# Kernel optimization log

Hardware: AMD Instinct MI355X
Metric: run time of the kernel (lower is better)

The kernel has to match this reference:

```python
import jax, jax.numpy as jnp
import numpy as np

N_NODES = 50000
N_EDGES = 800000


def gat_conv(x, src, dst, ea, W, We, a_s, a_d, a_e, b, n_nodes):
    """PyG GATConv with edge_dim, add_self_loops=True, fill_value='mean', concat=True."""
    H, C = a_s.shape
    dt = x.dtype
    # self-loop edge_attr = mean of incoming edge attrs per destination node
    deg = jax.ops.segment_sum(jnp.ones((src.shape[0],), dt), dst, num_segments=n_nodes)
    loop_attr = jax.ops.segment_sum(ea, dst, num_segments=n_nodes) / jnp.clip(deg, 1.0)[:, None]
    nodes = jnp.arange(n_nodes, dtype=src.dtype)
    s = jnp.concatenate([src, nodes])
    d = jnp.concatenate([dst, nodes])
    e_attr = jnp.concatenate([ea, loop_attr], axis=0)       # [E2, edge_dim]
    h = (x @ W).reshape(n_nodes, H, C)                       # [N,H,C]
    e = (e_attr @ We).reshape(-1, H, C)                      # [E2,H,C]
    a_src = jnp.einsum('nhc,hc->nh', h, a_s)                 # [N,H]
    a_dst = jnp.einsum('nhc,hc->nh', h, a_d)
    a_edg = jnp.einsum('ehc,hc->eh', e, a_e)                 # [E2,H]
    lg = jax.nn.leaky_relu(a_src[s] + a_dst[d] + a_edg, 0.2)  # [E2,H]
    m = jax.ops.segment_max(lg, d, num_segments=n_nodes)     # every node has a self-loop
    p = jnp.exp(lg - m[d])
    z = jax.ops.segment_sum(p, d, num_segments=n_nodes)
    alpha = p / z[d]                                         # segment softmax over dst
    out = jax.ops.segment_sum(alpha[:, :, None] * h[s], d, num_segments=n_nodes)
    return out.reshape(n_nodes, H * C) + b


def setup_inputs() -> dict:
    key = jax.random.key(0)
    ks = iter(jax.random.split(key, 40))
    sc = 0.05
    inp = {
        'x': jax.random.normal(next(ks), (N_NODES, 128), jnp.float32),
        'edge_index': jax.random.randint(next(ks), (2, N_EDGES), 0, N_NODES, dtype=jnp.int32),
        'edge_attr': jax.random.uniform(next(ks), (N_EDGES, 1), jnp.float32),
        'fa_w': jax.random.normal(next(ks), (128, 128)) * sc, 'fa_b': jnp.zeros((128,)),
        'W1': jax.random.normal(next(ks), (128, 256)) * sc, 'We1': jax.random.normal(next(ks), (1, 256)) * sc,
        'as1': jax.random.normal(next(ks), (4, 64)) * sc, 'ad1': jax.random.normal(next(ks), (4, 64)) * sc,
        'ae1': jax.random.normal(next(ks), (4, 64)) * sc, 'b1': jnp.zeros((256,)),
        'W2': jax.random.normal(next(ks), (256, 256)) * sc, 'We2': jax.random.normal(next(ks), (1, 256)) * sc,
        'as2': jax.random.normal(next(ks), (4, 64)) * sc, 'ad2': jax.random.normal(next(ks), (4, 64)) * sc,
        'ae2': jax.random.normal(next(ks), (4, 64)) * sc, 'b2': jnp.zeros((256,)),
        'W3': jax.random.normal(next(ks), (256, 64)) * sc, 'We3': jax.random.normal(next(ks), (1, 64)) * sc,
        'as3': jax.random.normal(next(ks), (1, 64)) * sc, 'ad3': jax.random.normal(next(ks), (1, 64)) * sc,
        'ae3': jax.random.normal(next(ks), (1, 64)) * sc, 'b3': jnp.zeros((64,)),
        'r1_w': jax.random.normal(next(ks), (128, 256)) * sc, 'r1_b': jnp.zeros((256,)),
        'r2_w': jax.random.normal(next(ks), (256, 256)) * sc, 'r2_b': jnp.zeros((256,)),
        'ffn_w1': jax.random.normal(next(ks), (128, 64)) * sc, 'ffn_b1': jnp.zeros((64,)),
        'ffn_w2': jax.random.normal(next(ks), (64, 64)) * sc, 'ffn_b2': jnp.zeros((64,)),
    }
    return inp


def reference(x, edge_index, edge_attr, fa_w, fa_b,
              W1, We1, as1, ad1, ae1, b1,
              W2, We2, as2, ad2, ae2, b2,
              W3, We3, as3, ad3, ae3, b3,
              r1_w, r1_b, r2_w, r2_b,
              ffn_w1, ffn_b1, ffn_w2, ffn_b2):
    n = x.shape[0]
    src, dst = edge_index[0], edge_index[1]
    # feature attention gate
    x = x * jax.nn.sigmoid(x @ fa_w + fa_b)
    xr1 = x @ r1_w + r1_b
    z1 = gat_conv(x, src, dst, edge_attr, W1, We1, as1, ad1, ae1, b1, n)
    z1 = jax.nn.leaky_relu(z1, 0.01) + xr1          # dropout = identity (eval)
    z2 = gat_conv(z1, src, dst, edge_attr, W2, We2, as2, ad2, ae2, b2, n)
    z2 = jax.nn.leaky_relu(z2, 0.01) + (z1 @ r2_w + r2_b)
    z3 = gat_conv(z2, src, dst, edge_attr, W3, We3, as3, ad3, ae3, b3, n)
    z_self = jax.nn.relu(x @ ffn_w1 + ffn_b1) @ ffn_w2 + ffn_b2
    z3 = jax.nn.leaky_relu(z3, 0.01) + z_self
    return z3
```

## Files before the change

### kernel.cpp

```cpp
#include <hip/hip_runtime.h>
#include <hip/hip_bf16.h>


typedef unsigned short u16;
typedef unsigned int   u32;
typedef __attribute__((ext_vector_type(8))) short short8;
typedef __attribute__((ext_vector_type(4))) float float4v;

typedef const __attribute__((address_space(1))) u32* gptr_t;
typedef __attribute__((address_space(3))) u32* lptr_t;
#define GLOAD_LDS16(g, l) \
    __builtin_amdgcn_global_load_lds((gptr_t)(const void*)(g), (lptr_t)(void*)(l), 16, 0, 0)

static __device__ __forceinline__ u16 f2b(float f) {
    u32 u = __float_as_uint(f);
    u32 r = u + 0x7fffu + ((u >> 16) & 1u);
    return (u16)(r >> 16);
}
static __device__ __forceinline__ float b2f(u16 u) {
    return __uint_as_float(((u32)u) << 16);
}
static __device__ __forceinline__ float lo2f(u32 v) { return __uint_as_float(v << 16); }
static __device__ __forceinline__ float hi2f(u32 v) { return __uint_as_float(v & 0xffff0000u); }
static __device__ __forceinline__ float lrelu02(float x) { return fmaxf(x, 0.2f * x); }

__global__ void prep_mega(const float* __restrict__ x, u16* __restrict__ xb, int n4,
                          const float* s0, const float* s1, const float* s2,
                          const float* s3, const float* s4, const float* s5,
                          const float* s6, const float* s7,
                          u16* d0, u16* d1, u16* d2, u16* d3,
                          u16* d4, u16* d5, u16* d6, u16* d7,
                          const float* We1, const float* ae1,
                          const float* We2, const float* ae2,
                          const float* We3, const float* ae3, float* ce_g) {
    int role = blockIdx.y;
    if (role == 0) {
        int i = blockIdx.x * 256 + threadIdx.x;
        if (i >= n4) return;
        float4 v = ((const float4*)x)[i];
        ushort4 o;
        o.x = f2b(v.x); o.y = f2b(v.y); o.z = f2b(v.z); o.w = f2b(v.w);
        ((ushort4*)xb)[i] = o;
    } else {
        int wid = blockIdx.x >> 4, sub = blockIdx.x & 15;
        if (wid > 8) return;
        if (wid == 8) {
            if (sub == 0) {
                int t = threadIdx.x;
                if (t < 9) {
                    const float* W; const float* a; int h;
                    if (t < 4)      { W = We1; a = ae1; h = t; }
                    else if (t < 8) { W = We2; a = ae2; h = t - 4; }
                    else            { W = We3; a = ae3; h = 0; }
                    float s = 0.f;
                    for (int c = 0; c < 64; c++) s += W[h * 64 + c] * a[h * 64 + c];
                    ce_g[t] = s;
                }
            }
            return;
        }
        const float* src; u16* dst; int K, N;
        switch (wid) {
            case 0: src = s0; dst = d0; K = 128; N = 128; break;
            case 1: src = s1; dst = d1; K = 128; N = 256; break;
            case 2: src = s2; dst = d2; K = 128; N = 256; break;
            case 3: src = s3; dst = d3; K = 256; N = 256; break;
            case 4: src = s4; dst = d4; K = 256; N = 256; break;
            case 5: src = s5; dst = d5; K = 256; N = 64;  break;
            case 6: src = s6; dst = d6; K = 128; N = 64;  break;
            default: src = s7; dst = d7; K = 64;  N = 64;  break;
        }
        int KN = K * N;
        int nmask = N - 1;
        int nshift = __popc((u32)nmask);
        for (int i = sub * 256 + threadIdx.x; i < KN; i += 16 * 256) {
            int k = i >> nshift, n2 = i & nmask;
            dst[(size_t)n2 * K + k] = f2b(src[i]);
        }
    }
}

__global__ void scan_block_kernel(const u32* __restrict__ deg, int* incl,
                                  int* blocksum, int Nn) {
    __shared__ int sb[256];
    int t = threadIdx.x;
    int n = blockIdx.x * 256 + t;
    int v = (n < Nn) ? (int)deg[n] : 0;
    sb[t] = v;
    __syncthreads();
    for (int off = 1; off < 256; off <<= 1) {
        int x = (t >= off) ? sb[t - off] : 0;
        __syncthreads();
        sb[t] += x;
        __syncthreads();
    }
    if (n < Nn) incl[n] = sb[t];
    if (t == 255) blocksum[blockIdx.x] = sb[255];
}

__global__ void scan_final_kernel(const u32* __restrict__ deg, const int* __restrict__ incl,
                                  const int* __restrict__ blocksum,
                                  int* row_ptr, int Nn) {
    __shared__ int sb[256];
    int t = threadIdx.x;
    int b = blockIdx.x;
    sb[t] = (t < b) ? blocksum[t] : 0;
    __syncthreads();
    for (int off = 128; off > 0; off >>= 1) {
        if (t < off) sb[t] += sb[t + off];
        __syncthreads();
    }
    int base = sb[0];
    int n = b * 256 + t;
    if (n >= Nn) return;
    int d = (int)deg[n];
    int excl = base + incl[n] - d;
    row_ptr[n] = excl;
    if (n == Nn - 1) row_ptr[Nn] = excl + d;
}

#define LDSS 40
__global__ __launch_bounds__(256)
void fa_atomic_kernel(const u16* __restrict__ A, const u16* __restrict__ Bt,
                      const float* __restrict__ bias, const u16* __restrict__ extraB,
                      u16* __restrict__ Cb,
                      const int* __restrict__ ei, u32* deg, u32* rank, int E, int nx) {
    int gid = blockIdx.x;
    int role = gid % 3;
    int idx = gid / 3;
    if (role == 2) {
        for (int e = idx * 256 + threadIdx.x; e < E; e += nx * 256)
            rank[e] = atomicAdd(&deg[ei[E + e]], 1u);
        return;
    }
    __shared__ u16 As[64 * LDSS];
    __shared__ u16 Bs[64 * LDSS];
    const int K = 128, N = 128;
    int t = threadIdx.x;
    int bm = idx * 64, bn = role * 64;
    int w = t >> 6, lane = t & 63;
    int wm = w & 1, wn = w >> 1;
    int lm = lane & 15, q = lane >> 4;

    float4v acc[2][2];
#pragma unroll
    for (int i = 0; i < 2; i++)
#pragma unroll
        for (int j = 0; j < 2; j++) acc[i][j] = (float4v){0.f, 0.f, 0.f, 0.f};

    int ar = t >> 2;
    int ac = (t & 3) * 8;
    const u16* aPtr = A + (size_t)(bm + ar) * K + ac;
    const u16* bPtr = Bt + (size_t)(bn + ar) * K + ac;

#pragma unroll
    for (int k0 = 0; k0 < K; k0 += 32) {
        uint4 av = *(const uint4*)(aPtr + k0);
        uint4 bv = *(const uint4*)(bPtr + k0);
        *(uint4*)&As[ar * LDSS + ac] = av;
        *(uint4*)&Bs[ar * LDSS + ac] = bv;
        __syncthreads();

        short8 fa0 = *(const short8*)&As[(32 * wm + lm) * LDSS + q * 8];
        short8 fa1 = *(const short8*)&As[(32 * wm + 16 + lm) * LDSS + q * 8];
        short8 fb0 = *(const short8*)&Bs[(32 * wn + lm) * LDSS + q * 8];
        short8 fb1 = *(const short8*)&Bs[(32 * wn + 16 + lm) * LDSS + q * 8];
        acc[0][0] = __builtin_amdgcn_mfma_f32_16x16x32_bf16(fa0, fb0, acc[0][0], 0, 0, 0);
        acc[0][1] = __builtin_amdgcn_mfma_f32_16x16x32_bf16(fa0, fb1, acc[0][1], 0, 0, 0);
        acc[1][0] = __builtin_amdgcn_mfma_f32_16x16x32_bf16(fa1, fb0, acc[1][0], 0, 0, 0);
        acc[1][1] = __builtin_amdgcn_mfma_f32_16x16x32_bf16(fa1, fb1, acc[1][1], 0, 0, 0);
        __syncthreads();
    }

#pragma unroll
    for (int i = 0; i < 2; i++)
#pragma unroll
        for (int j = 0; j < 2; j++) {
            int col = bn + 32 * wn + 16 * j + lm;
            float bval = bias[col];
#pragma unroll
            for (int r = 0; r < 4; r++) {
                int row = bm + 32 * wm + 16 * i + q * 4 + r;
                float v = acc[i][j][r] + bval;
                float xv = b2f(extraB[(size_t)row * N + col]);
                v = xv / (1.f + __expf(-v));
                Cb[(size_t)row * N + col] = f2b(v);
            }
        }
}

__global__ __launch_bounds__(256)
void c1_scatter_kernel(const u16* __restrict__ A, const u16* __restrict__ Bt,
                       const float* __restrict__ bias1, const float* __restrict__ bias2,
                       u16* __restrict__ Cres, u16* __restrict__ Ch, u16* __restrict__ Cmid,
                       const int* __restrict__ ei, const float* __restrict__ ea,
                       const int* __restrict__ row_ptr, const u32* __restrict__ rank,
                       int2* __restrict__ csr2, int E, int nx) {
    int gid = blockIdx.x;
    int role = gid % 6;
    int idx = gid / 6;
    if (role == 5) {
        for (int e = idx * 256 + threadIdx.x; e < E; e += nx * 256) {
            int d = ei[E + e];
            csr2[row_ptr[d] + (int)rank[e]] = make_int2(ei[e], __float_as_int(ea[e]));
        }
        return;
    }
    __shared__ u16 As[128 * 32];
    __shared__ u16 Bs[128 * 32];
    const int K = 128;
    int t = threadIdx.x;
    int w = t >> 6, lane = t & 63;
    int wm = w & 1, wn = w >> 1;
    int lm = lane & 15, q = lane >> 4;
    int bm = idx * 128, bn = role * 128;

    float4v acc[4][4];
#pragma unroll
    for (int i = 0; i < 4; i++)
#pragma unroll
        for (int j = 0; j < 4; j++) acc[i][j] = (float4v){0.f, 0.f, 0.f, 0.f};

    int srow = lane >> 2;
    int scol = (lane & 3) * 8;
    const u16* aG = A + (size_t)(bm + w * 32 + srow) * K + scol;
    const u16* bG = Bt + (size_t)(bn + w * 32 + srow) * K + scol;
    u16* aL0 = &As[(w * 32) * 32];
    u16* aL1 = &As[(w * 32 + 16) * 32];
    u16* bL0 = &Bs[(w * 32) * 32];
    u16* bL1 = &Bs[(w * 32 + 16) * 32];

#pragma unroll
    for (int k0 = 0; k0 < K; k0 += 32) {
        GLOAD_LDS16(aG + k0, aL0);
        GLOAD_LDS16(aG + (size_t)16 * K + k0, aL1);
        GLOAD_LDS16(bG + k0, bL0);
        GLOAD_LDS16(bG + (size_t)16 * K + k0, bL1);
        __syncthreads();

        short8 af[4], bf[4];
#pragma unroll
        for (int i = 0; i < 4; i++)
            af[i] = *(const short8*)&As[(64 * wm + 16 * i + lm) * 32 + q * 8];
#pragma unroll
        for (int j = 0; j < 4; j++)
            bf[j] = *(const short8*)&Bs[(64 * wn + 16 * j + lm) * 32 + q * 8];
#pragma unroll
        for (int i = 0; i < 4; i++)
#pragma unroll
            for (int j = 0; j < 4; j++)
                acc[i][j] = __builtin_amdgcn_mfma_f32_16x16x32_bf16(af[i], bf[j], acc[i][j], 0, 0, 0);
        __syncthreads();
    }

#pragma unroll
    for (int i = 0; i < 4; i++)
#pragma unroll
        for (int j = 0; j < 4; j++) {
            int col = bn + 64 * wn + 16 * j + lm;
#pragma unroll
            for (int r = 0; r < 4; r++) {
                int row = bm + 64 * wm + 16 * i + q * 4 + r;
                float v = acc[i][j][r];
                if (col < 256) {
                    Cres[(size_t)row * 256 + col] = f2b(v + bias1[col]);
                } else if (col < 512) {
                    Ch[(size_t)row * 256 + (col - 256)] = f2b(v);
                } else if (col < 576) {
                    Cmid[(size_t)row * 64 + (col - 512)] = f2b(fmaxf(v + bias2[col - 512], 0.f));
                }
            }
        }
}

template <int K>
__global__ __launch_bounds__(256)
void gemm128_kernel(const u16* __restrict__ A, const u16* __restrict__ Bt,
                    const float* __restrict__ bias1,
                    u16* __restrict__ Cres, u16* __restrict__ Ch) {
    __shared__ u16 As[128 * 32];
    __shared__ u16 Bs[128 * 32];
    int t = threadIdx.x;
    int w = t >> 6, lane = t & 63;
    int wm = w & 1, wn = w >> 1;
    int lm = lane & 15, q = lane >> 4;
    int bm = blockIdx.x * 128, bn = blockIdx.y * 128;

    float4v acc[4][4];
#pragma unroll
    for (int i = 0; i < 4; i++)
#pragma unroll
        for (int j = 0; j < 4; j++) acc[i][j] = (float4v){0.f, 0.f, 0.f, 0.f};

    int srow = lane >> 2;
    int scol = (lane & 3) * 8;
    const u16* aG = A + (size_t)(bm + w * 32 + srow) * K + scol;
    const u16* bG = Bt + (size_t)(bn + w * 32 + srow) * K + scol;
    u16* aL0 = &As[(w * 32) * 32];
    u16* aL1 = &As[(w * 32 + 16) * 32];
    u16* bL0 = &Bs[(w * 32) * 32];
    u16* bL1 = &Bs[(w * 32 + 16) * 32];

#pragma unroll
    for (int k0 = 0; k0 < K; k0 += 32) {
        GLOAD_LDS16(aG + k0, aL0);
        GLOAD_LDS16(aG + (size_t)16 * K + k0, aL1);
        GLOAD_LDS16(bG + k0, bL0);
        GLOAD_LDS16(bG + (size_t)16 * K + k0, bL1);
        __syncthreads();

        short8 af[4], bf[4];
#pragma unroll
        for (int i = 0; i < 4; i++)
            af[i] = *(const short8*)&As[(64 * wm + 16 * i + lm) * 32 + q * 8];
#pragma unroll
        for (int j = 0; j < 4; j++)
            bf[j] = *(const short8*)&Bs[(64 * wn + 16 * j + lm) * 32 + q * 8];
#pragma unroll
        for (int i = 0; i < 4; i++)
#pragma unroll
            for (int j = 0; j < 4; j++)
                acc[i][j] = __builtin_amdgcn_mfma_f32_16x16x32_bf16(af[i], bf[j], acc[i][j], 0, 0, 0);
        __syncthreads();
    }

#pragma unroll
    for (int i = 0; i < 4; i++)
#pragma unroll
        for (int j = 0; j < 4; j++) {
            int col = bn + 64 * wn + 16 * j + lm;
#pragma unroll
            for (int r = 0; r < 4; r++) {
                int row = bm + 64 * wm + 16 * i + q * 4 + r;
                float v = acc[i][j][r];
                if (col < 256) {
                    Cres[(size_t)row * 256 + col] = f2b(v + bias1[col]);
                } else {
                    Ch[(size_t)row * 256 + (col - 256)] = f2b(v);
                }
            }
        }
}

template <int EPI, int K>
__global__ __launch_bounds__(256)
void gemm_kernel(const u16* __restrict__ A, const u16* __restrict__ Bt,
                 const float* __restrict__ bias, u16* __restrict__ Cb, int N) {
    __shared__ u16 As[64 * LDSS];
    __shared__ u16 Bs[64 * LDSS];
    int t = threadIdx.x;
    int bm = blockIdx.x * 64, bn = blockIdx.y * 64;
    int w = t >> 6, lane = t & 63;
    int wm = w & 1, wn = w >> 1;
    int lm = lane & 15, q = lane >> 4;

    float4v acc[2][2];
#pragma unroll
    for (int i = 0; i < 2; i++)
#pragma unroll
        for (int j = 0; j < 2; j++) acc[i][j] = (float4v){0.f, 0.f, 0.f, 0.f};

    int ar = t >> 2;
    int ac = (t & 3) * 8;
    const u16* aPtr = A + (size_t)(bm + ar) * K + ac;
    const u16* bPtr = Bt + (size_t)(bn + ar) * K + ac;

#pragma unroll
    for (int k0 = 0; k0 < K; k0 += 32) {
        uint4 av = *(const uint4*)(aPtr + k0);
        uint4 bv = *(const uint4*)(bPtr + k0);
        *(uint4*)&As[ar * LDSS + ac] = av;
        *(uint4*)&Bs[ar * LDSS + ac] = bv;
        __syncthreads();

        short8 fa0 = *(const short8*)&As[(32 * wm + lm) * LDSS + q * 8];
        short8 fa1 = *(const short8*)&As[(32 * wm + 16 + lm) * LDSS + q * 8];
        short8 fb0 = *(const short8*)&Bs[(32 * wn + lm) * LDSS + q * 8];
        short8 fb1 = *(const short8*)&Bs[(32 * wn + 16 + lm) * LDSS + q * 8];
        acc[0][0] = __builtin_amdgcn_mfma_f32_16x16x32_bf16(fa0, fb0, acc[0][0], 0, 0, 0);
        acc[0][1] = __builtin_amdgcn_mfma_f32_16x16x32_bf16(fa0, fb1, acc[0][1], 0, 0, 0);
        acc[1][0] = __builtin_amdgcn_mfma_f32_16x16x32_bf16(fa1, fb0, acc[1][0], 0, 0, 0);
        acc[1][1] = __builtin_amdgcn_mfma_f32_16x16x32_bf16(fa1, fb1, acc[1][1], 0, 0, 0);
        __syncthreads();
    }

#pragma unroll
    for (int i = 0; i < 2; i++)
#pragma unroll
        for (int j = 0; j < 2; j++) {
            int col = bn + 32 * wn + 16 * j + lm;
            float bval = (EPI >= 1) ? bias[col] : 0.f;
#pragma unroll
            for (int r = 0; r < 4; r++) {
                int row = bm + 32 * wm + 16 * i + q * 4 + r;
                float v = acc[i][j][r] + bval;
                Cb[(size_t)row * N + col] = f2b(v);
            }
        }
}

__global__ __launch_bounds__(256)
void att4_kernel(const uint2* __restrict__ hb2, const float* __restrict__ a_s,
                 const float* __restrict__ a_d, float* att_s, float* att_d, int Nn) {
    int wv = threadIdx.x >> 6;
    int n = blockIdx.x * 4 + wv;
    if (n >= Nn) return;
    int lane = threadIdx.x & 63;
    float4 as4 = *(const float4*)&a_s[lane * 4];
    float4 ad4 = *(const float4*)&a_d[lane * 4];
    uint2 v = hb2[(size_t)n * 64 + lane];
    float c0 = lo2f(v.x), c1 = hi2f(v.x), c2 = lo2f(v.y), c3 = hi2f(v.y);
    float ps = c0 * as4.x + c1 * as4.y + c2 * as4.z + c3 * as4.w;
    float pd = c0 * ad4.x + c1 * ad4.y + c2 * ad4.z + c3 * ad4.w;
#pragma unroll
    for (int off = 8; off > 0; off >>= 1) {
        ps += __shfl_down(ps, off);
        pd += __shfl_down(pd, off);
    }
    if ((lane & 15) == 0) {
        att_s[n * 4 + (lane >> 4)] = ps;
        att_d[n * 4 + (lane >> 4)] = pd;
    }
}

__global__ __launch_bounds__(256)
void att1_kernel(const u32* __restrict__ hb, const float* __restrict__ a_s,
                 const float* __restrict__ a_d, float* att_s, float* att_d, int Nn) {
    int wv = threadIdx.x >> 6;
    int n = blockIdx.x * 4 + wv;
    if (n >= Nn) return;
    int lane = threadIdx.x & 63;
    int cl = lane & 31;
    float2 as2 = *(const float2*)&a_s[cl * 2];
    float2 ad2 = *(const float2*)&a_d[cl * 2];
    u32 v = hb[(u32)n * 32u + cl];
    float c0 = lo2f(v), c1 = hi2f(v);
    float ps = c0 * as2.x + c1 * as2.y;
    float pd = c0 * ad2.x + c1 * ad2.y;
    if (lane >= 32) { ps = 0.f; pd = 0.f; }
#pragma unroll
    for (int off = 16; off > 0; off >>= 1) {
        ps += __shfl_down(ps, off);
        pd += __shfl_down(pd, off);
    }
    if (lane == 0) {
        att_s[n] = ps;
        att_d[n] = pd;
    }
}

__global__ __launch_bounds__(256)
void agg4_kernel(const uint2* __restrict__ hb2,
                 const float* __restrict__ att_s, const float* __restrict__ att_d,
                 const int* __restrict__ row_ptr, const int2* __restrict__ csr2,
                 const float* __restrict__ ce_g, const float* __restrict__ bias,
                 const uint2* __restrict__ resid2, u16* __restrict__ outb, int Nn) {
    int wv = __builtin_amdgcn_readfirstlane(threadIdx.x >> 6);
    int n = blockIdx.x * 4 + wv;
    if (n >= Nn) return;
    int lane = threadIdx.x & 63;
    int hh = lane >> 4;

    float ce = ce_g[hh];
    float adn = att_d[n * 4 + hh];
    float asn = att_s[n * 4 + hh];
    uint2 sv = hb2[(size_t)n * 64 + lane];
    float z = 0.f, qsum = 0.f;
    float aA0 = 0.f, aA1 = 0.f, aA2 = 0.f, aA3 = 0.f;
    float aB0 = 0.f, aB1 = 0.f, aB2 = 0.f, aB3 = 0.f;

    int e0 = row_ptr[n], e1 = row_ptr[n + 1];
    for (int base = e0; base < e1; base += 64) {
        int cnt = min(64, e1 - base);
        int2 cc = csr2[base + min(lane, cnt - 1)];
        int vsrc = cc.x;
        float vea = __int_as_float(cc.y);
        int i = 0;
        for (; i + 4 <= cnt; i += 4) {
            int sA = __shfl(vsrc, i),     sB = __shfl(vsrc, i + 1);
            int sC = __shfl(vsrc, i + 2), sD = __shfl(vsrc, i + 3);
            float qA = __shfl(vea, i),     qB = __shfl(vea, i + 1);
            float qC = __shfl(vea, i + 2), qD = __shfl(vea, i + 3);
            float gA = att_s[(u32)sA * 4u + hh], gB = att_s[(u32)sB * 4u + hh];
            float gC = att_s[(u32)sC * 4u + hh], gD = att_s[(u32)sD * 4u + hh];
            uint2 vA = hb2[(u32)sA * 64u + lane], vB = hb2[(u32)sB * 64u + lane];
            uint2 vC = hb2[(u32)sC * 64u + lane], vD = hb2[(u32)sD * 64u + lane];
            float pA = __expf(lrelu02(gA + adn + qA * ce));
            float pB = __expf(lrelu02(gB + adn + qB * ce));
            float pC = __expf(lrelu02(gC + adn + qC * ce));
            float pD = __expf(lrelu02(gD + adn + qD * ce));
            qsum += (qA + qB) + (qC + qD);
            z += (pA + pB) + (pC + pD);
            aA0 = fmaf(pA, lo2f(vA.x), aA0); aA1 = fmaf(pA, hi2f(vA.x), aA1);
            aA2 = fmaf(pA, lo2f(vA.y), aA2); aA3 = fmaf(pA, hi2f(vA.y), aA3);
            aB0 = fmaf(pB, lo2f(vB.x), aB0); aB1 = fmaf(pB, hi2f(vB.x), aB1);
            aB2 = fmaf(pB, lo2f(vB.y), aB2); aB3 = fmaf(pB, hi2f(vB.y), aB3);
            aA0 = fmaf(pC, lo2f(vC.x), aA0); aA1 = fmaf(pC, hi2f(vC.x), aA1);
            aA2 = fmaf(pC, lo2f(vC.y), aA2); aA3 = fmaf(pC, hi2f(vC.y), aA3);
            aB0 = fmaf(pD, lo2f(vD.x), aB0); aB1 = fmaf(pD, hi2f(vD.x), aB1);
            aB2 = fmaf(pD, lo2f(vD.y), aB2); aB3 = fmaf(pD, hi2f(vD.y), aB3);
        }
        for (; i < cnt; i++) {
            int s = __shfl(vsrc, i);
            float q = __shfl(vea, i);
            float g = att_s[(u32)s * 4u + hh];
            uint2 v = hb2[(u32)s * 64u + lane];
            float p = __expf(lrelu02(g + adn + q * ce));
            qsum += q;
            z += p;
            aA0 = fmaf(p, lo2f(v.x), aA0); aA1 = fmaf(p, hi2f(v.x), aA1);
            aA2 = fmaf(p, lo2f(v.y), aA2); aA3 = fmaf(p, hi2f(v.y), aA3);
        }
    }
    float la = qsum / (float)max(e1 - e0, 1);
    float ps = __expf(lrelu02(asn + adn + la * ce));
    z += ps;
    float a0 = aA0 + aB0 + ps * lo2f(sv.x);
    float a1 = aA1 + aB1 + ps * hi2f(sv.x);
    float a2 = aA2 + aB2 + ps * lo2f(sv.y);
    float a3 = aA3 + aB3 + ps * hi2f(sv.y);

    float inv = 1.f / z;
    int c0 = lane * 4;
    float4 bv = *(const float4*)&bias[c0];
    uint2 rr = resid2[(size_t)n * 64 + lane];
    float o0 = fmaf(a0, inv, bv.x);
    float o1 = fmaf(a1, inv, bv.y);
    float o2 = fmaf(a2, inv, bv.z);
    float o3 = fmaf(a3, inv, bv.w);
    o0 = fmaxf(o0, 0.01f * o0) + lo2f(rr.x);
    o1 = fmaxf(o1, 0.01f * o1) + hi2f(rr.x);
    o2 = fmaxf(o2, 0.01f * o2) + lo2f(rr.y);
    o3 = fmaxf(o3, 0.01f * o3) + hi2f(rr.y);
    uint2 packed;
    packed.x = ((u32)f2b(o0)) | (((u32)f2b(o1)) << 16);
    packed.y = ((u32)f2b(o2)) | (((u32)f2b(o3)) << 16);
    ((uint2*)outb)[(size_t)n * 64 + lane] = packed;
}

__global__ __launch_bounds__(256)
void agg1_kernel(const uint2* __restrict__ hb2,
                 const float* __restrict__ att_s, const float* __restrict__ att_d,
                 const int* __restrict__ row_ptr, const int2* __restrict__ csr2,
                 const float* __restrict__ ce_g, const float* __restrict__ bias,
                 const uint2* __restrict__ zs2, float* __restrict__ outf, int Nn) {
    int wv = __builtin_amdgcn_readfirstlane(threadIdx.x >> 6);
    int n = blockIdx.x * 4 + wv;
    if (n >= Nn) return;
    int lane = threadIdx.x & 63;
    int qtr = lane >> 4;
    int cl = lane & 15;

    float ce = ce_g[8];
    float adn = att_d[n];
    float asn = att_s[n];
    uint2 sv = hb2[(u32)n * 16u + cl];
    float z = 0.f, qsum = 0.f;
    float a0 = 0.f, a1 = 0.f, a2 = 0.f, a3 = 0.f;

    int e0 = row_ptr[n], e1 = row_ptr[n + 1];
    for (int base = e0; base < e1; base += 64) {
        int cnt = min(64, e1 - base);
        int2 cc = csr2[base + min(lane, cnt - 1)];
        int vsrc = cc.x;
        float vea = __int_as_float(cc.y);
        for (int i = 0; i < cnt; i += 4) {
            int idx = min(i + qtr, cnt - 1);
            int s = __shfl(vsrc, idx);
            float q = __shfl(vea, idx);
            bool act = (i + qtr < cnt);
            float p = __expf(lrelu02(att_s[s] + adn + q * ce));
            p = act ? p : 0.f;
            q = act ? q : 0.f;
            uint2 v = hb2[(u32)s * 16u + cl];
            z += p;
            qsum += q;
            a0 = fmaf(p, lo2f(v.x), a0);
            a1 = fmaf(p, hi2f(v.x), a1);
            a2 = fmaf(p, lo2f(v.y), a2);
            a3 = fmaf(p, hi2f(v.y), a3);
        }
    }
    z += __shfl_xor(z, 16);       z += __shfl_xor(z, 32);
    qsum += __shfl_xor(qsum, 16); qsum += __shfl_xor(qsum, 32);
    a0 += __shfl_xor(a0, 16);     a0 += __shfl_xor(a0, 32);
    a1 += __shfl_xor(a1, 16);     a1 += __shfl_xor(a1, 32);
    a2 += __shfl_xor(a2, 16);     a2 += __shfl_xor(a2, 32);
    a3 += __shfl_xor(a3, 16);     a3 += __shfl_xor(a3, 32);

    float la = qsum / (float)max(e1 - e0, 1);
    float ps = __expf(lrelu02(asn + adn + la * ce));
    z += ps;
    a0 += ps * lo2f(sv.x);
    a1 += ps * hi2f(sv.x);
    a2 += ps * lo2f(sv.y);
    a3 += ps * hi2f(sv.y);

    if (lane < 16) {
        float inv = 1.f / z;
        int c0 = cl * 4;
        float4 bv = *(const float4*)&bias[c0];
        uint2 zz = zs2[(u32)n * 16u + cl];
        float o0 = fmaf(a0, inv, bv.x);
        float o1 = fmaf(a1, inv, bv.y);
        float o2 = fmaf(a2, inv, bv.z);
        float o3 = fmaf(a3, inv, bv.w);
        o0 = fmaxf(o0, 0.01f * o0) + lo2f(zz.x);
        o1 = fmaxf(o1, 0.01f * o1) + hi2f(zz.x);
        o2 = fmaxf(o2, 0.01f * o2) + lo2f(zz.y);
        o3 = fmaxf(o3, 0.01f * o3) + hi2f(zz.y);
        *(float4*)&outf[(size_t)n * 64 + c0] = make_float4(o0, o1, o2, o3);
    }
}

extern "C" void kernel_launch(void* const* d_in, const int* in_sizes, int n_in,
                              void* d_out, int out_size, void* d_ws, size_t ws_size,
                              hipStream_t stream) {
    const float* x    = (const float*)d_in[0];
    const int*   ei   = (const int*)d_in[1];
    const float* ea   = (const float*)d_in[2];
    const float* fa_w = (const float*)d_in[3];
    const float* fa_b = (const float*)d_in[4];
    const float* W1   = (const float*)d_in[5];
    const float* We1  = (const float*)d_in[6];
    const float* as1  = (const float*)d_in[7];
    const float* ad1  = (const float*)d_in[8];
    const float* ae1  = (const float*)d_in[9];
    const float* b1   = (const float*)d_in[10];
    const float* W2   = (const float*)d_in[11];
    const float* We2  = (const float*)d_in[12];
    const float* as2  = (const float*)d_in[13];
    const float* ad2  = (const float*)d_in[14];
    const float* ae2  = (const float*)d_in[15];
    const float* b2   = (const float*)d_in[16];
    const float* W3   = (const float*)d_in[17];
    const float* We3  = (const float*)d_in[18];
    const float* as3  = (const float*)d_in[19];
    const float* ad3  = (const float*)d_in[20];
    const float* ae3  = (const float*)d_in[21];
    const float* b3   = (const float*)d_in[22];
    const float* r1_w = (const float*)d_in[23];
    const float* r1_b = (const float*)d_in[24];
    const float* r2_w = (const float*)d_in[25];
    const float* r2_b = (const float*)d_in[26];
    const float* fw1  = (const float*)d_in[27];
    const float* fb1  = (const float*)d_in[28];
    const float* fw2  = (const float*)d_in[29];
    const float* fb2  = (const float*)d_in[30];

    const int Nn = in_sizes[0] / 128;
    const int E  = in_sizes[1] / 2;

    char* ws = (char*)d_ws;
    size_t off = 0;
    auto alloc = [&](size_t bytes) -> char* {
        char* p = ws + off;
        off += (bytes + 255) & ~((size_t)255);
        return p;
    };
    u32*   deg      = (u32*)alloc((size_t)Nn * 4);
    u32*   rank     = (u32*)alloc((size_t)E * 4);
    int*   incl     = (int*)alloc((size_t)Nn * 4);
    int*   row_ptr  = (int*)alloc((size_t)(Nn + 1) * 4);
    int*   blocksum = (int*)alloc(1024);
    float* att_s    = (float*)alloc((size_t)Nn * 16);
    float* att_d    = (float*)alloc((size_t)Nn * 16);
    int2*  csr2     = (int2*)alloc((size_t)E * 8);
    float* ce_g     = (float*)alloc(64);
    u16* xbf   = (u16*)alloc((size_t)(Nn + 128) * 128 * 2);
    u16* xg_bf = (u16*)alloc((size_t)(Nn + 128) * 128 * 2);
    u16* h_bf  = (u16*)alloc((size_t)(Nn + 128) * 256 * 2);
    u16* z_bf  = (u16*)alloc((size_t)(Nn + 128) * 256 * 2);
    u16* mid_bf = (u16*)alloc((size_t)(Nn + 128) * 64 * 2);
    u16* h3_bf  = (u16*)alloc((size_t)(Nn + 128) * 64 * 2);
    u16* wt_fa = (u16*)alloc(16384 * 2);
    u16* wt_c1 = (u16*)alloc((size_t)640 * 128 * 2);
    u16* wt_c2 = (u16*)alloc((size_t)512 * 256 * 2);
    u16* wt_W3 = (u16*)alloc(16384 * 2);
    u16* wt_f2 = (u16*)alloc(4096 * 2);
    u16* residB = (u16*)alloc((size_t)(Nn + 128) * 256 * 2);
    u16* zself  = (u16*)alloc((size_t)(Nn + 128) * 64 * 2);

    hipMemsetAsync(deg, 0, (size_t)Nn * 4, stream);

    int nb = (Nn + 255) / 256;
    int n4 = Nn * 128 / 4;
    int xb4 = (n4 + 255) / 256;

    prep_mega<<<dim3(xb4, 2), 256, 0, stream>>>(
        x, xbf, n4,
        fa_w, r1_w, W1, r2_w, W2, W3, fw1, fw2,
        wt_fa, wt_c1, wt_c1 + (size_t)256 * 128, wt_c2, wt_c2 + (size_t)256 * 256,
        wt_W3, wt_c1 + (size_t)512 * 128, wt_f2, We1, ae1, We2, ae2, We3, ae3, ce_g);

    int mb  = (Nn + 63) / 64;
    int mb1 = (Nn + 127) / 128;
    int ab  = (Nn + 3) / 4;

    fa_atomic_kernel<<<mb * 3, 256, 0, stream>>>(xbf, wt_fa, fa_b, xbf, xg_bf,
                                                 ei, deg, rank, E, mb);
    scan_block_kernel<<<nb, 256, 0, stream>>>(deg, incl, blocksum, Nn);
    scan_final_kernel<<<nb, 256, 0, stream>>>(deg, incl, blocksum, row_ptr, Nn);
    c1_scatter_kernel<<<mb1 * 6, 256, 0, stream>>>(xg_bf, wt_c1, r1_b, fb1,
                                                   residB, h_bf, mid_bf,
                                                   ei, ea, row_ptr, rank, csr2, E, mb1);
    att4_kernel<<<ab, 256, 0, stream>>>((const uint2*)h_bf, as1, ad1, att_s, att_d, Nn);
    agg4_kernel<<<ab, 256, 0, stream>>>((const uint2*)h_bf, att_s, att_d, row_ptr, csr2,
                                        ce_g, b1, (const uint2*)residB, z_bf, Nn);
    gemm128_kernel<256><<<dim3(mb1, 4), 256, 0, stream>>>(z_bf, wt_c2, r2_b, residB, h_bf);
    att4_kernel<<<ab, 256, 0, stream>>>((const uint2*)h_bf, as2, ad2, att_s, att_d, Nn);
    agg4_kernel<<<ab, 256, 0, stream>>>((const uint2*)h_bf, att_s, att_d, row_ptr, csr2,
                                        ce_g + 4, b2, (const uint2*)residB, z_bf, Nn);
    gemm_kernel<1, 64><<<dim3(mb, 1), 256, 0, stream>>>(mid_bf, wt_f2, fb2, zself, 64);
    gemm_kernel<0, 256><<<dim3(mb, 1), 256, 0, stream>>>(z_bf, wt_W3, nullptr, h3_bf, 64);
    att1_kernel<<<ab, 256, 0, stream>>>((const u32*)h3_bf, as3, ad3, att_s, att_d, Nn);
    agg1_kernel<<<ab, 256, 0, stream>>>((const uint2*)h3_bf, att_s, att_d, row_ptr, csr2,
                                        ce_g, b3, (const uint2*)zself, (float*)d_out, Nn);
}
```

Measured before the change: 487.3 us.

## Pad degree counters, add more atomic/scatter blocks, fuse FFN2 GEMM into layer-2 GEMM

Degree counters are spread 64 bytes apart so the atomic increments for different destination nodes no longer share cache lines, and the scan kernels read them with the same stride. The atomic-count and CSR-scatter roles get twice and three times as many blocks inside the fused GEMM kernels. The small FFN second-layer GEMM is folded into the layer-2 GEMM launch as an extra grid column, which removes one kernel launch. The cost is a 16x larger degree buffer and memset, and a strided, less efficient read pattern in the scan.

```diff
diff --git a/kernel.cpp b/kernel.cpp
--- a/kernel.cpp
+++ b/kernel.cpp
@@ -85,7 +85,7 @@
     __shared__ int sb[256];
     int t = threadIdx.x;
     int n = blockIdx.x * 256 + t;
-    int v = (n < Nn) ? (int)deg[n] : 0;
+    int v = (n < Nn) ? (int)deg[(u32)n * 16u] : 0;
     sb[t] = v;
     __syncthreads();
     for (int off = 1; off < 256; off <<= 1) {
@@ -113,7 +113,7 @@
     int base = sb[0];
     int n = b * 256 + t;
     if (n >= Nn) return;
-    int d = (int)deg[n];
+    int d = (int)deg[(u32)n * 16u];
     int excl = base + incl[n] - d;
     row_ptr[n] = excl;
     if (n == Nn - 1) row_ptr[Nn] = excl + d;
@@ -126,11 +126,12 @@
                       u16* __restrict__ Cb,
                       const int* __restrict__ ei, u32* deg, u32* rank, int E, int nx) {
     int gid = blockIdx.x;
-    int role = gid % 3;
-    int idx = gid / 3;
-    if (role == 2) {
-        for (int e = idx * 256 + threadIdx.x; e < E; e += nx * 256)
-            rank[e] = atomicAdd(&deg[ei[E + e]], 1u);
+    int role = gid & 3;
+    int idx = gid >> 2;
+    if (role >= 2) {
+        int sid = idx * 2 + (role - 2);
+        for (int e = sid * 256 + threadIdx.x; e < E; e += nx * 2 * 256)
+            rank[e] = atomicAdd(&deg[(u32)ei[E + e] * 16u], 1u);
         return;
     }
     __shared__ u16 As[64 * LDSS];
@@ -197,10 +198,11 @@
                        const int* __restrict__ row_ptr, const u32* __restrict__ rank,
                        int2* __restrict__ csr2, int E, int nx) {
     int gid = blockIdx.x;
-    int role = gid % 6;
-    int idx = gid / 6;
-    if (role == 5) {
-        for (int e = idx * 256 + threadIdx.x; e < E; e += nx * 256) {
+    int role = gid & 7;
+    int idx = gid >> 3;
+    if (role >= 5) {
+        int sid = idx * 3 + (role - 5);
+        for (int e = sid * 256 + threadIdx.x; e < E; e += nx * 3 * 256) {
             int d = ei[E + e];
             csr2[row_ptr[d] + (int)rank[e]] = make_int2(ei[e], __float_as_int(ea[e]));
         }
@@ -273,19 +275,67 @@
         }
 }
 
-template <int K>
 __global__ __launch_bounds__(256)
-void gemm128_kernel(const u16* __restrict__ A, const u16* __restrict__ Bt,
-                    const float* __restrict__ bias1,
-                    u16* __restrict__ Cres, u16* __restrict__ Ch) {
+void c2f2_kernel(const u16* __restrict__ A, const u16* __restrict__ Bt,
+                 const float* __restrict__ bias1,
+                 u16* __restrict__ Cres, u16* __restrict__ Ch,
+                 const u16* __restrict__ Am, const u16* __restrict__ Bf2,
+                 const float* __restrict__ fb2, u16* __restrict__ zself) {
     __shared__ u16 As[128 * 32];
     __shared__ u16 Bs[128 * 32];
     int t = threadIdx.x;
     int w = t >> 6, lane = t & 63;
     int wm = w & 1, wn = w >> 1;
     int lm = lane & 15, q = lane >> 4;
+
+    if (blockIdx.y == 4) {
+        int bm = blockIdx.x * 128;
+        float4v acc[4][2];
+#pragma unroll
+        for (int i = 0; i < 4; i++)
+#pragma unroll
+            for (int j = 0; j < 2; j++) acc[i][j] = (float4v){0.f, 0.f, 0.f, 0.f};
+        int ar = t >> 2;
+        int ac = (t & 3) * 8;
+        const u16* aP = Am + (size_t)(bm + ar) * 64 + ac;
+        const u16* bP = Bf2 + (size_t)ar * 64 + ac;
+#pragma unroll
+        for (int k0 = 0; k0 < 64; k0 += 32) {
+            *(uint4*)&As[ar * 32 + ac] = *(const uint4*)(aP + k0);
+            *(uint4*)&As[(64 + ar) * 32 + ac] = *(const uint4*)(aP + (size_t)64 * 64 + k0);
+            *(uint4*)&Bs[ar * 32 + ac] = *(const uint4*)(bP + k0);
+            __syncthreads();
+            short8 af[4], bfv[2];
+#pragma unroll
+            for (int i = 0; i < 4; i++)
+                af[i] = *(const short8*)&As[(64 * wm + 16 * i + lm) * 32 + q * 8];
+#pragma unroll
+            for (int j = 0; j < 2; j++)
+                bfv[j] = *(const short8*)&Bs[(32 * wn + 16 * j + lm) * 32 + q * 8];
+#pragma unroll
+            for (int i = 0; i < 4; i++)
+#pragma unroll
+                for (int j = 0; j < 2; j++)
+                    acc[i][j] = __builtin_amdgcn_mfma_f32_16x16x32_bf16(af[i], bfv[j], acc[i][j], 0, 0, 0);
+            __syncthreads();
+        }
+#pragma unroll
+        for (int i = 0; i < 4; i++)
+#pragma unroll
+            for (int j = 0; j < 2; j++) {
+                int col = 32 * wn + 16 * j + lm;
+                float bval = fb2[col];
+#pragma unroll
+                for (int r = 0; r < 4; r++) {
+                    int row = bm + 64 * wm + 16 * i + q * 4 + r;
+                    zself[(size_t)row * 64 + col] = f2b(acc[i][j][r] + bval);
+                }
+            }
+        return;
+    }
+
+    const int K = 256;
     int bm = blockIdx.x * 128, bn = blockIdx.y * 128;
-
     float4v acc[4][4];
 #pragma unroll
     for (int i = 0; i < 4; i++)
@@ -658,7 +708,7 @@
         off += (bytes + 255) & ~((size_t)255);
         return p;
     };
-    u32*   deg      = (u32*)alloc((size_t)Nn * 4);
+    u32*   deg      = (u32*)alloc((size_t)Nn * 64);
     u32*   rank     = (u32*)alloc((size_t)E * 4);
     int*   incl     = (int*)alloc((size_t)Nn * 4);
     int*   row_ptr  = (int*)alloc((size_t)(Nn + 1) * 4);
@@ -681,7 +731,7 @@
     u16* residB = (u16*)alloc((size_t)(Nn + 128) * 256 * 2);
     u16* zself  = (u16*)alloc((size_t)(Nn + 128) * 64 * 2);
 
-    hipMemsetAsync(deg, 0, (size_t)Nn * 4, stream);
+    hipMemsetAsync(deg, 0, (size_t)Nn * 64, stream);
 
     int nb = (Nn + 255) / 256;
     int n4 = Nn * 128 / 4;
@@ -697,21 +747,21 @@
     int mb1 = (Nn + 127) / 128;
     int ab  = (Nn + 3) / 4;
 
-    fa_atomic_kernel<<<mb * 3, 256, 0, stream>>>(xbf, wt_fa, fa_b, xbf, xg_bf,
+    fa_atomic_kernel<<<mb * 4, 256, 0, stream>>>(xbf, wt_fa, fa_b, xbf, xg_bf,
                                                  ei, deg, rank, E, mb);
     scan_block_kernel<<<nb, 256, 0, stream>>>(deg, incl, blocksum, Nn);
     scan_final_kernel<<<nb, 256, 0, stream>>>(deg, incl, blocksum, row_ptr, Nn);
-    c1_scatter_kernel<<<mb1 * 6, 256, 0, stream>>>(xg_bf, wt_c1, r1_b, fb1,
+    c1_scatter_kernel<<<mb1 * 8, 256, 0, stream>>>(xg_bf, wt_c1, r1_b, fb1,
                                                    residB, h_bf, mid_bf,
                                                    ei, ea, row_ptr, rank, csr2, E, mb1);
     att4_kernel<<<ab, 256, 0, stream>>>((const uint2*)h_bf, as1, ad1, att_s, att_d, Nn);
     agg4_kernel<<<ab, 256, 0, stream>>>((const uint2*)h_bf, att_s, att_d, row_ptr, csr2,
                                         ce_g, b1, (const uint2*)residB, z_bf, Nn);
-    gemm128_kernel<256><<<dim3(mb1, 4), 256, 0, stream>>>(z_bf, wt_c2, r2_b, residB, h_bf);
+    c2f2_kernel<<<dim3(mb1, 5), 256, 0, stream>>>(z_bf, wt_c2, r2_b, residB, h_bf,
+                                                  mid_bf, wt_f2, fb2, zself);
     att4_kernel<<<ab, 256, 0, stream>>>((const uint2*)h_bf, as2, ad2, att_s, att_d, Nn);
     agg4_kernel<<<ab, 256, 0, stream>>>((const uint2*)h_bf, att_s, att_d, row_ptr, csr2,
                                         ce_g + 4, b2, (const uint2*)residB, z_bf, Nn);
-    gemm_kernel<1, 64><<<dim3(mb, 1), 256, 0, stream>>>(mid_bf, wt_f2, fb2, zself, 64);
     gemm_kernel<0, 256><<<dim3(mb, 1), 256, 0, stream>>>(z_bf, wt_W3, nullptr, h3_bf, 64);
     att1_kernel<<<ab, 256, 0, stream>>>((const u32*)h3_bf, as3, ad3, att_s, att_d, Nn);
     agg1_kernel<<<ab, 256, 0, stream>>>((const uint2*)h3_bf, att_s, att_d, row_ptr, csr2,
```

Result: no change. 494.7 us (+1.5%).
